# Kernel optimization log

Hardware: AMD Instinct MI355X
Metric: run time of the kernel (lower is better)

## Reference

```python
import jax, jax.numpy as jnp
import numpy as np

B, T, D, R, WP, WF, NS = 32, 256, 512, 4, 8, 8, 2
N = B * T


def _build_graph():
    # Windowed dialog graph: edge j -> i for j in [i-WP, i+WF], j != i.
    # rel = (0 if same speaker else 2) + (1 if j > i else 0)
    rng = np.random.RandomState(0)
    spk = rng.randint(0, NS, size=(B, T))
    src, dst, rel = [], [], []
    for b in range(B):
        off = b * T
        for i in range(T):
            for j in range(max(0, i - WP), min(T - 1, i + WF) + 1):
                if j == i:
                    continue
                r = (0 if spk[b, j] == spk[b, i] else 2) + int(j > i)
                src.append(off + j)
                dst.append(off + i)
                rel.append(r)
    return np.array([src, dst], dtype=np.int32), np.array(rel, dtype=np.int32)


def setup_inputs() -> dict:
    key = jax.random.key(0)
    ks = jax.random.split(key, 16)
    ei, et = _build_graph()
    s = 0.02
    f32 = jnp.float32
    return {
        "x": jax.random.normal(ks[0], (B, T, D), f32),
        "edge_index": jnp.asarray(ei),
        "edge_type": jnp.asarray(et),
        # RGCNConv params (aggr='mean', root_weight=True, bias=True)
        "W_rel": jax.random.normal(ks[1], (R, D, D), f32) * s,
        "W_root": jax.random.normal(ks[2], (D, D), f32) * s,
        "b_rgcn": jnp.zeros((D,), f32),
        # TransformerConv params (heads=1, concat=True, root_weight=True)
        "Wq": jax.random.normal(ks[3], (D, D), f32) * s,
        "bq": jnp.zeros((D,), f32),
        "Wk": jax.random.normal(ks[4], (D, D), f32) * s,
        "bk": jnp.zeros((D,), f32),
        "Wv": jax.random.normal(ks[5], (D, D), f32) * s,
        "bv": jnp.zeros((D,), f32),
        "Wskip": jax.random.normal(ks[6], (D, D), f32) * s,
        "bskip": jnp.zeros((D,), f32),
        # LayerNorm params
        "gamma": jnp.ones((D,), f32),
        "beta": jnp.zeros((D,), f32),
    }


def _gnn(x, edge_index, edge_type, W_rel, W_root, b_rgcn,
         Wq, bq, Wk, bk, Wv, bv, Wskip, bskip, gamma, beta):
    nodes = x.reshape(N, D)  # all dia_len == T, so valid nodes = all nodes
    src, dst = edge_index[0], edge_index[1]

    # --- RGCNConv: per-relation linear + mean aggregation over each relation ---
    xW = jnp.einsum("nd,rde->nre", nodes, W_rel)          # [N, R, D]
    msg = xW[src, edge_type]                                # [E, D]
    comb = dst * R + edge_type                              # group (dst, rel)
    cnt = jax.ops.segment_sum(jnp.ones(src.shape, nodes.dtype), comb,
                              num_segments=N * R).reshape(N, R)
    inv = 1.0 / jnp.maximum(cnt, 1.0)
    msg = msg * inv[dst, edge_type][:, None]
    ho = jax.ops.segment_sum(msg, dst, num_segments=N) + nodes @ W_root + b_rgcn

    # --- TransformerConv (heads=1): edge attention + scatter-softmax ---
    q = ho @ Wq + bq
    k = ho @ Wk + bk
    v = ho @ Wv + bv
    logits = jnp.sum(q[dst] * k[src], axis=-1) / jnp.sqrt(jnp.asarray(D, ho.dtype))
    mx = jax.ops.segment_max(logits, dst, num_segments=N)
    mx = jnp.where(jnp.isfinite(mx), mx, 0.0)               # nodes w/o in-edges
    ex = jnp.exp(logits - mx[dst])
    den = jax.ops.segment_sum(ex, dst, num_segments=N)
    alpha = ex / jnp.maximum(den[dst], 1e-16)
    agg = jax.ops.segment_sum(alpha[:, None] * v[src], dst, num_segments=N)
    h = agg + ho @ Wskip + bskip

    h = jax.nn.leaky_relu(h, 0.01)                          # dropout = identity (eval)
    out = x + h.reshape(B, T, D)
    mu = out.mean(-1, keepdims=True)
    var = out.var(-1, keepdims=True)
    return (out - mu) / jnp.sqrt(var + 1e-5) * gamma + beta


def reference(x, edge_index, edge_type, W_rel, W_root, b_rgcn,
              Wq, bq, Wk, bk, Wv, bv, Wskip, bskip, gamma, beta):
    out = _gnn(x, edge_index, edge_type, W_rel, W_root, b_rgcn,
               Wq, bq, Wk, bk, Wv, bv, Wskip, bskip, gamma, beta)
    return out, jnp.asarray(0.0, x.dtype)  # graph_cl_loss == 0 in eval path
```

## Files before the change

### kernel.cpp

```cpp
#include <hip/hip_runtime.h>

typedef unsigned short u16;
typedef __attribute__((ext_vector_type(8))) short s16x8;
typedef __attribute__((ext_vector_type(4))) float f32x4;

__device__ __forceinline__ float bf2f(u16 u) {
  union { unsigned int i; float f; } v; v.i = ((unsigned int)u) << 16; return v.f;
}
__device__ __forceinline__ u16 f2bf(float f) {
  union { float f; unsigned int i; } v; v.f = f;
  unsigned int r = (v.i + 0x7FFFu + ((v.i >> 16) & 1u)) >> 16;
  return (u16)r;
}
__device__ __forceinline__ void async16(const void* g, void* l) {
  __builtin_amdgcn_global_load_lds((const __attribute__((address_space(1))) void*)g,
                                   (__attribute__((address_space(3))) void*)l, 16, 0, 0);
}

__global__ __launch_bounds__(256) void prep_kernel(
    const float* __restrict__ W_rel, const float* __restrict__ W_root,
    const float* __restrict__ Wq, const float* __restrict__ Wk,
    const float* __restrict__ Wv, const float* __restrict__ Wskip,
    const float* __restrict__ bq, const float* __restrict__ bk,
    const float* __restrict__ bv, const float* __restrict__ bskip,
    const float* __restrict__ x,
    u16* __restrict__ Bt1, u16* __restrict__ Bt2, float* __restrict__ bias2,
    u16* __restrict__ Acat, int Nn,
    const int* __restrict__ dst, int E, int* __restrict__ rs, int* __restrict__ re)
{
  const int b = (int)blockIdx.x;
  const int tid = threadIdx.x;
  if (b < 576) {
    __shared__ float tile[64][65];
    const float* S;
    u16* D;
    int ldD;
    long dbase;
    if (b < 320) {
      const int kt = b >> 3, et = b & 7;
      const int r0 = kt * 64, c0 = et * 64;
      S = (r0 < 2048) ? (W_rel + (long)r0 * 512 + c0)
                      : (W_root + (long)(r0 - 2048) * 512 + c0);
      D = Bt1; ldD = 2560; dbase = (long)c0 * 2560 + r0;
    } else {
      const int b2 = b - 320;
      const int jt = b2 >> 3, kt = b2 & 7;
      const int j0 = jt * 64, k0 = kt * 64;
      const int which = j0 >> 9, col0 = j0 & 511;
      const float* W = (which == 0) ? Wq : (which == 1) ? Wk : (which == 2) ? Wv : Wskip;
      S = W + (long)k0 * 512 + col0;
      D = Bt2; ldD = 512; dbase = (long)j0 * 512 + k0;
    }
    const int lc = tid & 63;
#pragma unroll
    for (int i = 0; i < 16; ++i) {
      const int r = (tid >> 6) * 16 + i;
      tile[r][lc] = S[(long)r * 512 + lc];
    }
    __syncthreads();
    const int oc2 = (tid & 31) * 2;
#pragma unroll
    for (int i = 0; i < 8; ++i) {
      const int orow = (tid >> 5) + i * 8;
      const unsigned int pk = (unsigned int)f2bf(tile[oc2][orow]) |
                              ((unsigned int)f2bf(tile[oc2 + 1][orow]) << 16);
      *(unsigned int*)(D + dbase + (long)orow * ldD + oc2) = pk;
    }
  } else if (b == 576) {
#pragma unroll
    for (int i = 0; i < 8; ++i) {
      const int j = tid + i * 256;
      const int which = j >> 9, col = j & 511;
      const float* bb = (which == 0) ? bq : (which == 1) ? bk : (which == 2) ? bv : bskip;
      bias2[j] = bb[col];
    }
  } else if (b < 8769) {
    const long u = ((long)(b - 577) * 256 + tid) * 2;
    if (u < (long)Nn * 512) {
      const float2 v = *(const float2*)(x + u);
      const unsigned int pk = (unsigned int)f2bf(v.x) | ((unsigned int)f2bf(v.y) << 16);
      *(unsigned int*)(Acat + ((long)(u >> 9)) * 2560 + 2048 + (u & 511)) = pk;
    }
  } else {
    const int e = (b - 8769) * 256 + tid;
    if (e < E) {
      const int d = dst[e];
      if (e == 0 || dst[e - 1] != d) rs[d] = e;
      if (e == E - 1 || dst[e + 1] != d) re[d] = e + 1;
    }
  }
}

__global__ __launch_bounds__(256) void aggregate_kernel(
    const float* __restrict__ x, const int* __restrict__ src,
    const int* __restrict__ etype, const int* __restrict__ rs,
    const int* __restrict__ re, u16* __restrict__ Acat)
{
  __shared__ int s_src[16];
  __shared__ int s_rel[16];
  const int q = (int)gridDim.x >> 3;
  const int bid = (int)blockIdx.x;
  const int i = (bid & 7) * q + (bid >> 3);
  const int tid = threadIdx.x;
  const int s = rs[i];
  int nE = re[i] - s;
  if (nE > 16) nE = 16;
  if (tid < nE) { s_src[tid] = src[s + tid]; s_rel[tid] = etype[s + tid]; }
  __syncthreads();

  float2 acc[4] = {};
  int cnt[4] = {0, 0, 0, 0};
  for (int t = 0; t < nE; ++t) {
    const int sj = s_src[t];
    const int rel = s_rel[t];
    const float2 v = *(const float2*)(x + (long)sj * 512 + tid * 2);
#pragma unroll
    for (int r = 0; r < 4; ++r)
      if (rel == r) { acc[r].x += v.x; acc[r].y += v.y; cnt[r]++; }
  }

  const long base = (long)i * 2560 + tid * 2;
#pragma unroll
  for (int r = 0; r < 4; ++r) {
    const float inv = 1.0f / fmaxf((float)cnt[r], 1.0f);
    const unsigned int pk = ((unsigned int)f2bf(acc[r].y * inv) << 16) | f2bf(acc[r].x * inv);
    *(unsigned int*)(Acat + base + r * 512) = pk;
  }
}

__global__ __launch_bounds__(512) void gemm_bt_kernel(
    const u16* __restrict__ A, const u16* __restrict__ Bt,
    const float* __restrict__ bias, u16* __restrict__ C,
    const int M, const int N, const int K)
{
  __shared__ u16 lds[3][2][128 * 64];
  const int tid = threadIdx.x;
  const int lane = tid & 63, wid = tid >> 6;
  const int nbn = N >> 7;
  const int q = (int)gridDim.x >> 3;
  const int bid = (int)blockIdx.x;
  const int swz = (bid & 7) * q + (bid >> 3);
  const int bm = swz / nbn, bn = swz % nbn;
  const int wr = wid >> 2, wc = wid & 3;

  f32x4 acc[4][2] = {};

  const int srow = tid >> 3;
  const int sch = tid & 7;
  const long a_row0 = (long)bm * 128;
  const long b_row0 = (long)bn * 128;
  const int lds_wbase = wid * 512;

  auto STAGE = [&](int buf, int kt) {
#pragma unroll
    for (int it = 0; it < 2; ++it) {
      const int row = it * 64 + srow;
      const int lch = sch ^ (row & 7);
      async16(A  + (a_row0 + row) * K + kt + lch * 8, &lds[buf][0][it * 4096 + lds_wbase]);
      async16(Bt + (b_row0 + row) * K + kt + lch * 8, &lds[buf][1][it * 4096 + lds_wbase]);
    }
  };

  const int nt = K >> 6;
  STAGE(0, 0);
  STAGE(1, 64);
  int bufc = 0;
  for (int t = 0; t < nt; ++t) {
    if (t + 1 < nt) { asm volatile("s_waitcnt vmcnt(4)" ::: "memory"); }
    else            { asm volatile("s_waitcnt vmcnt(0)" ::: "memory"); }
    __builtin_amdgcn_s_barrier();
    if (t + 2 < nt) {
      const int sb = (bufc == 0) ? 2 : bufc - 1;
      STAGE(sb, (t + 2) << 6);
    }
#pragma unroll
    for (int kk = 0; kk < 2; ++kk) {
      s16x8 af[4], bfr[2];
#pragma unroll
      for (int mi = 0; mi < 4; ++mi) {
        const int row = wr * 64 + mi * 16 + (lane & 15);
        const int cb = (kk * 64 + ((lane >> 4) << 4)) ^ ((row & 7) << 4);
        af[mi] = *(const s16x8*)((const char*)&lds[bufc][0][0] + row * 128 + cb);
      }
#pragma unroll
      for (int ni = 0; ni < 2; ++ni) {
        const int row = wc * 32 + ni * 16 + (lane & 15);
        const int cb = (kk * 64 + ((lane >> 4) << 4)) ^ ((row & 7) << 4);
        bfr[ni] = *(const s16x8*)((const char*)&lds[bufc][1][0] + row * 128 + cb);
      }
      __builtin_amdgcn_s_setprio(1);
#pragma unroll
      for (int mi = 0; mi < 4; ++mi)
#pragma unroll
        for (int ni = 0; ni < 2; ++ni)
          acc[mi][ni] = __builtin_amdgcn_mfma_f32_16x16x32_bf16(af[mi], bfr[ni], acc[mi][ni], 0, 0, 0);
      __builtin_amdgcn_s_setprio(0);
    }
    bufc = (bufc == 2) ? 0 : bufc + 1;
  }

#pragma unroll
  for (int mi = 0; mi < 4; ++mi) {
    const int row0 = bm * 128 + wr * 64 + mi * 16 + ((lane >> 4) << 2);
#pragma unroll
    for (int ni = 0; ni < 2; ++ni) {
      const int col = bn * 128 + wc * 32 + ni * 16 + (lane & 15);
      const float bv = bias[col];
#pragma unroll
      for (int j = 0; j < 4; ++j)
        C[(long)(row0 + j) * N + col] = f2bf(acc[mi][ni][j] + bv);
    }
  }
}

__global__ __launch_bounds__(256) void attn_tile_kernel(
    const u16* __restrict__ qkvs, const int* __restrict__ src,
    const int* __restrict__ rs, const int* __restrict__ re,
    const float* __restrict__ x, const float* __restrict__ gamma,
    const float* __restrict__ beta, float* __restrict__ out,
    float* __restrict__ scl)
{
  __shared__ u16 Kl[48 * 512];
  __shared__ u16 Vl[48 * 512];
  __shared__ float sm[32][16];
  __shared__ int s_src[32][16];
  __shared__ int s_s0[32];
  __shared__ int s_ne[32];
  const int bid = (int)blockIdx.x;
  const int tid = threadIdx.x;
  const int lane = tid & 63, wid = tid >> 6;
  const int tile = (bid & 7) * ((int)gridDim.x >> 3) + (bid >> 3);
  const int i0 = tile * 32;
  if (bid == 0 && tid == 0) scl[0] = 0.0f;

  const int blo = i0 & ~255;
  const int lo = max(i0 - 8, blo);
  const int hi = min(i0 + 40, blo + 256);
  const int R = hi - lo;

  if (tid < 32) {
    const int s0 = rs[i0 + tid];
    int ne = re[i0 + tid] - s0;
    if (ne > 16) ne = 16;
    s_s0[tid] = s0;
    s_ne[tid] = ne;
  }
  __syncthreads();
  for (int idx = tid; idx < 512; idx += 256) {
    const int d = idx >> 4, e = idx & 15;
    if (e < s_ne[d]) s_src[d][e] = src[s_s0[d] + e] - lo;
  }
#pragma unroll
  for (int k = 0; k < 12; ++k) {
    const int r = wid * 12 + k;
    if (r < R) {
      const long gb = (long)(lo + r) * 2048;
      async16(qkvs + gb + 512  + ((lane ^ (r & 3)) * 8), &Kl[r * 512 + lane * 8]);
      async16(qkvs + gb + 1024 + lane * 8,               &Vl[r * 512 + lane * 8]);
    }
  }
  asm volatile("s_waitcnt vmcnt(0)" ::: "memory");
  __syncthreads();

  const int g16 = lane & 15;
  const int eg  = lane >> 4;

#pragma unroll 1
  for (int j = 0; j < 8; ++j) {
    const int d = wid * 8 + j;
    const int i = i0 + d;
    const int ne = s_ne[d];
    float qv[32];
#pragma unroll
    for (int c = 0; c < 4; ++c) {
      const s16x8 q8 = *(const s16x8*)(qkvs + (long)i * 2048 + c * 128 + g16 * 8);
#pragma unroll
      for (int u = 0; u < 8; ++u) qv[c * 8 + u] = bf2f((u16)q8[u]);
    }
#pragma unroll
    for (int round = 0; round < 4; ++round) {
      const int e = round * 4 + eg;
      float dp = 0.f;
      if (e < ne) {
        const int r = s_src[d][e];
        const int rx = r & 3;
#pragma unroll
        for (int c = 0; c < 4; ++c) {
          const s16x8 k8 = *(const s16x8*)&Kl[r * 512 + (((c * 16 + g16) ^ rx) * 8)];
#pragma unroll
          for (int u = 0; u < 8; ++u) dp += qv[c * 8 + u] * bf2f((u16)k8[u]);
        }
      }
#pragma unroll
      for (int m = 1; m <= 8; m <<= 1) dp += __shfl_xor(dp, m);
      if (g16 == 0 && e < ne) sm[d][e] = dp * 0.04419417382415922f;
    }
    {
      const float v = (lane < 16 && lane < ne) ? sm[d][lane] : -1e30f;
      float mx = v;
#pragma unroll
      for (int m = 1; m <= 8; m <<= 1) mx = fmaxf(mx, __shfl_xor(mx, m));
      const float ex = (lane < 16 && lane < ne) ? expf(v - mx) : 0.f;
      float den = ex;
#pragma unroll
      for (int m = 1; m <= 8; m <<= 1) den += __shfl_xor(den, m);
      if (lane < 16 && lane < ne) sm[d][lane] = ex / fmaxf(den, 1e-16f);
    }
  }

  const int d8 = lane * 8;
#pragma unroll 1
  for (int j = 0; j < 8; ++j) {
    const int d = wid * 8 + j;
    const int i = i0 + d;
    const int ne = s_ne[d];
    float a[8] = {};
    for (int e = 0; e < ne; ++e) {
      const float al = sm[d][e];
      const int r = s_src[d][e];
      const s16x8 v8 = *(const s16x8*)&Vl[r * 512 + d8];
#pragma unroll
      for (int u = 0; u < 8; ++u) a[u] += al * bf2f((u16)v8[u]);
    }
    const s16x8 sk8 = *(const s16x8*)(qkvs + (long)i * 2048 + 1536 + d8);
    const float4 x0 = *(const float4*)(x + (long)i * 512 + d8);
    const float4 x1 = *(const float4*)(x + (long)i * 512 + d8 + 4);
    float o[8];
    float s = 0.f, s2 = 0.f;
#pragma unroll
    for (int u = 0; u < 8; ++u) {
      float h = a[u] + bf2f((u16)sk8[u]);
      h = (h > 0.f) ? h : 0.01f * h;
      const float xx = (u < 4) ? ((const float*)&x0)[u] : ((const float*)&x1)[u - 4];
      o[u] = xx + h;
      s += o[u];
      s2 += o[u] * o[u];
    }
#pragma unroll
    for (int m = 32; m >= 1; m >>= 1) { s += __shfl_xor(s, m); s2 += __shfl_xor(s2, m); }
    const float mean = s * (1.f / 512.f);
    const float var = s2 * (1.f / 512.f) - mean * mean;
    const float rstd = rsqrtf(var + 1e-5f);
    const float4 g0 = *(const float4*)(gamma + d8), g1 = *(const float4*)(gamma + d8 + 4);
    const float4 b0 = *(const float4*)(beta + d8),  b1 = *(const float4*)(beta + d8 + 4);
    float4 r0, r1;
    r0.x = (o[0] - mean) * rstd * g0.x + b0.x;
    r0.y = (o[1] - mean) * rstd * g0.y + b0.y;
    r0.z = (o[2] - mean) * rstd * g0.z + b0.z;
    r0.w = (o[3] - mean) * rstd * g0.w + b0.w;
    r1.x = (o[4] - mean) * rstd * g1.x + b1.x;
    r1.y = (o[5] - mean) * rstd * g1.y + b1.y;
    r1.z = (o[6] - mean) * rstd * g1.z + b1.z;
    r1.w = (o[7] - mean) * rstd * g1.w + b1.w;
    *(float4*)(out + (long)i * 512 + d8) = r0;
    *(float4*)(out + (long)i * 512 + d8 + 4) = r1;
  }
}

extern "C" void kernel_launch(void* const* d_in, const int* in_sizes, int n_in,
                              void* d_out, int out_size, void* d_ws, size_t ws_size,
                              hipStream_t stream) {
  const float* x      = (const float*)d_in[0];
  const int*   ei     = (const int*)d_in[1];
  const int*   et     = (const int*)d_in[2];
  const float* W_rel  = (const float*)d_in[3];
  const float* W_root = (const float*)d_in[4];
  const float* b_rgcn = (const float*)d_in[5];
  const float* Wq     = (const float*)d_in[6];
  const float* bq     = (const float*)d_in[7];
  const float* Wk     = (const float*)d_in[8];
  const float* bk     = (const float*)d_in[9];
  const float* Wv     = (const float*)d_in[10];
  const float* bv     = (const float*)d_in[11];
  const float* Wskip  = (const float*)d_in[12];
  const float* bskip  = (const float*)d_in[13];
  const float* gamma  = (const float*)d_in[14];
  const float* beta   = (const float*)d_in[15];
  const int E  = in_sizes[2];
  const int Nn = in_sizes[0] / 512;
  const int* srcA = ei;
  const int* dstA = ei + E;

  char* p = (char*)d_ws;
  u16* Acat   = (u16*)p;   p += (size_t)Nn * 2560 * 2;
  u16* Bt1    = (u16*)p;   p += (size_t)512 * 2560 * 2;
  u16* Bt2    = (u16*)p;   p += (size_t)2048 * 512 * 2;
  float* bias2= (float*)p; p += (size_t)2048 * 4;
  u16* ho     = (u16*)p;   p += (size_t)Nn * 512 * 2;
  u16* qkvs   = (u16*)p;   p += (size_t)Nn * 2048 * 2;
  int* rs     = (int*)p;   p += (size_t)Nn * 4;
  int* re     = (int*)p;   p += (size_t)Nn * 4;

  {
    const int FB = (E + 255) / 256;
    const int blocks = 8769 + FB;
    prep_kernel<<<blocks, 256, 0, stream>>>(W_rel, W_root, Wq, Wk, Wv, Wskip,
                                            bq, bk, bv, bskip, x, Bt1, Bt2, bias2, Acat, Nn,
                                            dstA, E, rs, re);
  }
  aggregate_kernel<<<Nn, 256, 0, stream>>>(x, srcA, et, rs, re, Acat);
  gemm_bt_kernel<<<(Nn / 128) * (512 >> 7), 512, 0, stream>>>(Acat, Bt1, b_rgcn, ho, Nn, 512, 2560);
  gemm_bt_kernel<<<(Nn / 128) * (2048 >> 7), 512, 0, stream>>>(ho, Bt2, bias2, qkvs, Nn, 2048, 512);
  attn_tile_kernel<<<Nn / 32, 256, 0, stream>>>(qkvs, srcA, rs, re, x, gamma, beta,
                                                (float*)d_out, (float*)d_out + (size_t)Nn * 512);
}
```

Measured before the change: 133.5 us.

## Add 256x256 tiled MFMA GEMM for the QKV-skip projection

Adds a new bf16 MFMA GEMM kernel with 256x256 output tiles, double-buffered async LDS loads with XOR swizzle, and per-wave 128x64 sub-tiles, and uses it for the ho x [Wq|Wk|Wv|Wskip] projection. Larger tiles raise arithmetic intensity and cut redundant global loads of A and B compared with the 128x128 kernel. The trade-off is fewer blocks (256 for N=8192, M=2048), which is close to the CU count and may leave some CUs underused. It also uses 128 KB of LDS and many accumulator registers per block.

Result: faster. 129.2 us (-3.3%).

```diff
diff --git a/kernel.cpp b/kernel.cpp
--- a/kernel.cpp
+++ b/kernel.cpp
@@ -213,6 +213,102 @@
   }
 }
 
+__global__ __launch_bounds__(512, 2) void gemm256_kernel(
+    const u16* __restrict__ A, const u16* __restrict__ Bt,
+    const float* __restrict__ bias, u16* __restrict__ C,
+    const int M, const int N, const int K)
+{
+  __shared__ u16 lds[2][2][256 * 64];
+  const int tid = threadIdx.x;
+  const int lane = tid & 63, wid = tid >> 6;
+  const int nbn = N >> 8;
+  const int q = (int)gridDim.x >> 3;
+  const int bid = (int)blockIdx.x;
+  const int swz = (bid & 7) * q + (bid >> 3);
+  const int bm = swz / nbn, bn = swz % nbn;
+  const int wr = wid >> 2, wc = wid & 3;
+
+  f32x4 acc[8][4] = {};
+
+  const int srow = tid >> 3;
+  const int sch = tid & 7;
+  const long a_row0 = (long)bm * 256;
+  const long b_row0 = (long)bn * 256;
+  const int lds_wbase = wid * 512;
+
+  auto STAGE = [&](int buf, int kt) {
+#pragma unroll
+    for (int it = 0; it < 4; ++it) {
+      const int row = it * 64 + srow;
+      const int lch = sch ^ (srow & 7);
+      async16(A  + (a_row0 + row) * K + kt + lch * 8, &lds[buf][0][it * 4096 + lds_wbase]);
+      async16(Bt + (b_row0 + row) * K + kt + lch * 8, &lds[buf][1][it * 4096 + lds_wbase]);
+    }
+  };
+
+  const int nt = K >> 6;
+  STAGE(0, 0);
+  int cur = 0;
+  for (int t = 0; t < nt; ++t) {
+    asm volatile("s_waitcnt vmcnt(0)" ::: "memory");
+    __builtin_amdgcn_s_barrier();
+    s16x8 bfr[4][2];
+#pragma unroll
+    for (int p = 0; p < 4; ++p) {
+      s16x8 af[2][2];
+#pragma unroll
+      for (int i2 = 0; i2 < 2; ++i2) {
+        const int row = wr * 128 + (p * 2 + i2) * 16 + (lane & 15);
+#pragma unroll
+        for (int kk = 0; kk < 2; ++kk) {
+          const int cb = (kk * 64 + ((lane >> 4) << 4)) ^ ((row & 7) << 4);
+          af[i2][kk] = *(const s16x8*)((const char*)&lds[cur][0][0] + row * 128 + cb);
+        }
+      }
+      if (p == 0) {
+#pragma unroll
+        for (int ni = 0; ni < 4; ++ni) {
+          const int row = wc * 64 + ni * 16 + (lane & 15);
+#pragma unroll
+          for (int kk = 0; kk < 2; ++kk) {
+            const int cb = (kk * 64 + ((lane >> 4) << 4)) ^ ((row & 7) << 4);
+            bfr[ni][kk] = *(const s16x8*)((const char*)&lds[cur][1][0] + row * 128 + cb);
+          }
+        }
+        if (t + 1 < nt) STAGE(cur ^ 1, (t + 1) << 6);
+      }
+      __builtin_amdgcn_s_barrier();
+      asm volatile("s_waitcnt lgkmcnt(0)" ::: "memory");
+      __builtin_amdgcn_sched_barrier(0);
+      __builtin_amdgcn_s_setprio(1);
+#pragma unroll
+      for (int i2 = 0; i2 < 2; ++i2)
+#pragma unroll
+        for (int ni = 0; ni < 4; ++ni)
+#pragma unroll
+          for (int kk = 0; kk < 2; ++kk)
+            acc[p * 2 + i2][ni] = __builtin_amdgcn_mfma_f32_16x16x32_bf16(
+                af[i2][kk], bfr[ni][kk], acc[p * 2 + i2][ni], 0, 0, 0);
+      __builtin_amdgcn_s_setprio(0);
+      __builtin_amdgcn_s_barrier();
+    }
+    cur ^= 1;
+  }
+
+#pragma unroll
+  for (int mi = 0; mi < 8; ++mi) {
+    const int row0 = bm * 256 + wr * 128 + mi * 16 + ((lane >> 4) << 2);
+#pragma unroll
+    for (int ni = 0; ni < 4; ++ni) {
+      const int col = bn * 256 + wc * 64 + ni * 16 + (lane & 15);
+      const float bv = bias[col];
+#pragma unroll
+      for (int j = 0; j < 4; ++j)
+        C[(long)(row0 + j) * N + col] = f2bf(acc[mi][ni][j] + bv);
+    }
+  }
+}
+
 __global__ __launch_bounds__(256) void attn_tile_kernel(
     const u16* __restrict__ qkvs, const int* __restrict__ src,
     const int* __restrict__ rs, const int* __restrict__ re,
@@ -400,7 +496,7 @@
   }
   aggregate_kernel<<<Nn, 256, 0, stream>>>(x, srcA, et, rs, re, Acat);
   gemm_bt_kernel<<<(Nn / 128) * (512 >> 7), 512, 0, stream>>>(Acat, Bt1, b_rgcn, ho, Nn, 512, 2560);
-  gemm_bt_kernel<<<(Nn / 128) * (2048 >> 7), 512, 0, stream>>>(ho, Bt2, bias2, qkvs, Nn, 2048, 512);
+  gemm256_kernel<<<(Nn / 256) * (2048 >> 8), 512, 0, stream>>>(ho, Bt2, bias2, qkvs, Nn, 2048, 512);
   attn_tile_kernel<<<Nn / 32, 256, 0, stream>>>(qkvs, srcA, rs, re, x, gamma, beta,
                                                 (float*)d_out, (float*)d_out + (size_t)Nn * 512);
 }
```
